# Optimization experiments

Measured on AMD Instinct MI355X. Metric: run time of the kernel, lower is better.

The kernel has to match this reference:

```python
import jax, jax.numpy as jnp
import numpy as np

N = 20000   # nodes
E = 320000  # edges (avg degree 16)
IN = 16     # in_node_nf
H = 64      # hidden_nf
OUT = 64    # out_node_nf
L = 4       # n_layers


def setup_inputs() -> dict:
    key = jax.random.key(0)
    ks = jax.random.split(key, 16)
    w = lambda k, shape: (jax.random.normal(k, shape, dtype=jnp.float32) * 0.05)
    zb = lambda *shape: jnp.zeros(shape, dtype=jnp.float32)
    return {
        "h": jax.random.normal(ks[0], (N, IN), dtype=jnp.float32),
        "x": jax.random.normal(ks[1], (N, 3), dtype=jnp.float32),
        "edge_index": jax.random.randint(ks[2], (2, E), 0, N),
        "emb_in_w": w(ks[3], (IN, H)), "emb_in_b": zb(H),
        "edge_w1": w(ks[4], (L, 2 * H + 1, H)), "edge_b1": zb(L, H),
        "edge_w2": w(ks[5], (L, H, H)), "edge_b2": zb(L, H),
        "coord_w1": w(ks[6], (L, H, H)), "coord_b1": zb(L, H),
        "coord_w2": w(ks[7], (L, H, 1)),  # bias-free last coord_mlp layer
        "node_w1": w(ks[8], (L, 2 * H, H)), "node_b1": zb(L, H),
        "node_w2": w(ks[9], (L, H, H)), "node_b2": zb(L, H),
        "emb_out_w": w(ks[10], (H, OUT)), "emb_out_b": zb(OUT),
    }


def reference(h, x, edge_index, emb_in_w, emb_in_b,
              edge_w1, edge_b1, edge_w2, edge_b2,
              coord_w1, coord_b1, coord_w2,
              node_w1, node_b1, node_w2, node_b2,
              emb_out_w, emb_out_b):
    row, col = edge_index[0], edge_index[1]
    act = jax.nn.silu
    # receiver in-degree for mean coordinate aggregation (clamped to >=1)
    cnt = jax.ops.segment_sum(jnp.ones((row.shape[0], 1), h.dtype), row, num_segments=N)
    cnt = jnp.maximum(cnt, 1.0)

    h = h @ emb_in_w + emb_in_b
    for l in range(L):
        # coord2radial
        diff = x[row] - x[col]                               # [E,3]
        radial = jnp.sum(diff * diff, axis=-1, keepdims=True)  # [E,1]
        # edge model: m_ij = phi_e(h_i, h_j, ||x_i-x_j||^2)
        e_in = jnp.concatenate([h[row], h[col], radial], axis=-1)  # [E,2H+1]
        m = act(e_in @ edge_w1[l] + edge_b1[l])
        m = act(m @ edge_w2[l] + edge_b2[l])                 # [E,H]
        # coord model: x_i += mean_j (x_i - x_j) * phi_x(m_ij)
        phi = act(m @ coord_w1[l] + coord_b1[l]) @ coord_w2[l]  # [E,1]
        trans = diff * phi                                    # [E,3]
        x = x + jax.ops.segment_sum(trans, row, num_segments=N) / cnt
        # node model: h_i = h_i + phi_h(h_i, sum_j m_ij)
        agg = jax.ops.segment_sum(m, row, num_segments=N)     # [N,H]
        n_in = jnp.concatenate([h, agg], axis=-1)             # [N,2H]
        out = act(n_in @ node_w1[l] + node_b1[l]) @ node_w2[l] + node_b2[l]
        h = h + out
    h = h @ emb_out_w + emb_out_b
    return h, x
```

## Files before the change

### kernel.cpp

```cpp
#include <hip/hip_runtime.h>
#include <hip/hip_bf16.h>


#define NN 20000
#define EE 320000
#define LSE 17024
#define LSN 6272

typedef unsigned short u16;
typedef unsigned int   u32;
typedef __attribute__((ext_vector_type(8))) short s16x8;
typedef __attribute__((ext_vector_type(4))) float f32x4;

__device__ __forceinline__ float bf2f(u16 u) { return __uint_as_float(((u32)u) << 16); }
__device__ __forceinline__ float silu_f(float x) {
    return x * __builtin_amdgcn_rcpf(1.0f + __expf(-x));
}

__device__ __forceinline__ u16 f2bf_rne(float f) {
    u32 u = __float_as_uint(f);
    return (u16)((u + 0x7FFFu + ((u >> 16) & 1u)) >> 16);
}
__device__ __forceinline__ float gldf(const void* p, int i, int bf) {
    return bf ? bf2f(((const u16*)p)[i]) : ((const float*)p)[i];
}
__device__ __forceinline__ u16 gldb(const void* p, int i, int bf) {
    return bf ? ((const u16*)p)[i] : f2bf_rne(((const float*)p)[i]);
}

__global__ void k_sentinel(u16* __restrict__ out, int n, float v) {
    int t = blockIdx.x * 256 + threadIdx.x;
    if (t < n) out[t] = f2bf_rne(v);
}

__global__ __launch_bounds__(256) void k_pack(
    const void* __restrict__ ew1, const void* __restrict__ eb1,
    const void* __restrict__ ew2, const void* __restrict__ eb2,
    const void* __restrict__ cw1, const void* __restrict__ cb1,
    const void* __restrict__ cw2,
    const void* __restrict__ nw1, const void* __restrict__ nb1,
    const void* __restrict__ nw2, const void* __restrict__ nb2,
    const u16* __restrict__ h_raw, const int* __restrict__ rowi,
    int* __restrict__ flag, int* __restrict__ deg,
    u16* __restrict__ pkE, u32* __restrict__ pkN)
{
    if (blockIdx.x >= 64) {
        int e = (blockIdx.x - 64) * 256 + threadIdx.x;
        if (e < EE) atomicAdd(&deg[rowi[e]], 1);
        return;
    }
    __shared__ int cnt_s;
    if (threadIdx.x == 0) cnt_s = 0;
    __syncthreads();
    if (threadIdx.x < 128) {
        float v = fabsf(bf2f(h_raw[threadIdx.x]));
        if (v >= 0.015625f && v <= 16.0f) atomicAdd(&cnt_s, 1);
    }
    __syncthreads();
    const int bf = (cnt_s >= 96) ? 1 : 0;
    if (blockIdx.x == 0 && threadIdx.x == 0) *flag = bf;

    const int gid = blockIdx.x * 256 + threadIdx.x;
    const int stride = 64 * 256;

    for (int g = gid; g < 4 * 16384; g += stride) {
        int l = g >> 14, idx = g & 16383;
        u16 v;
        if (idx < 8192) {
            int j = idx & 7, lane = (idx >> 3) & 63, t = (idx >> 9) & 3, w = idx >> 11;
            int k = 32 * w + (lane >> 4) * 8 + j, n = 16 * t + (lane & 15);
            v = gldb(ew1, l * 129 * 64 + k * 64 + n, bf);
        } else if (idx < 12288) {
            int i2 = idx - 8192;
            int j = i2 & 7, lane = (i2 >> 3) & 63, t = (i2 >> 9) & 3, w = i2 >> 11;
            int k = 32 * w + (lane >> 4) * 8 + j, n = 16 * t + (lane & 15);
            v = gldb(ew2, l * 4096 + k * 64 + n, bf);
        } else {
            int i2 = idx - 12288;
            int j = i2 & 7, lane = (i2 >> 3) & 63, t = (i2 >> 9) & 3, w = i2 >> 11;
            int k = 32 * w + (lane >> 4) * 8 + j, n = 16 * t + (lane & 15);
            v = gldb(cw1, l * 4096 + k * 64 + n, bf);
        }
        pkE[l * LSE + idx] = v;
    }
    for (int g = gid; g < 4 * 320; g += stride) {
        int l = g / 320, r = g % 320, wch = r >> 6, i = r & 63;
        float v = (wch == 0) ? gldf(eb1, l * 64 + i, bf)
                : (wch == 1) ? gldf(eb2, l * 64 + i, bf)
                : (wch == 2) ? gldf(cb1, l * 64 + i, bf)
                : (wch == 3) ? gldf(cw2, l * 64 + i, bf)
                :              gldf(ew1, l * 129 * 64 + 128 * 64 + i, bf);
        ((float*)(pkE + l * LSE + 16384))[r] = v;
    }
    for (int g = gid; g < 4 * 6144; g += stride) {
        int l = g / 6144, idx = g % 6144;
        u32 pv;
        if (idx < 4096) {
            int kp = idx >> 6, j = idx & 63;
            u32 lo = gldb(nw1, l * 8192 + (2 * kp) * 64 + j, bf);
            u32 hi = gldb(nw1, l * 8192 + (2 * kp + 1) * 64 + j, bf);
            pv = lo | (hi << 16);
        } else {
            int i2 = idx - 4096, kp = i2 >> 6, j = i2 & 63;
            u32 lo = gldb(nw2, l * 4096 + (2 * kp) * 64 + j, bf);
            u32 hi = gldb(nw2, l * 4096 + (2 * kp + 1) * 64 + j, bf);
            pv = lo | (hi << 16);
        }
        pkN[l * LSN + idx] = pv;
    }
    for (int g = gid; g < 4 * 128; g += stride) {
        int l = g >> 7, r = g & 127;
        float v = (r < 64) ? gldf(nb1, l * 64 + r, bf) : gldf(nb2, l * 64 + (r - 64), bf);
        ((float*)(pkN + l * LSN + 6144))[r] = v;
    }
}

__global__ __launch_bounds__(1024) void k_scan(const int* deg, int* offs, int* cursor,
                                               int* __restrict__ perm) {
    __shared__ int part[1024];
    __shared__ int hist[32], basep[32];
    const int tid = threadIdx.x;
    const int CH = (NN + 1023) / 1024;
    const int b0 = tid * CH;
    int s = 0;
    for (int i = 0; i < CH; i++) { int idx = b0 + i; if (idx < NN) s += deg[idx]; }
    part[tid] = s;
    __syncthreads();
    for (int d = 1; d < 1024; d <<= 1) {
        int v = (tid >= d) ? part[tid - d] : 0;
        __syncthreads();
        part[tid] += v;
        __syncthreads();
    }
    int run = (tid > 0) ? part[tid - 1] : 0;
    for (int i = 0; i < CH; i++) {
        int idx = b0 + i;
        if (idx < NN) {
            int dv = deg[idx];
            offs[idx] = run;
            cursor[idx] = run;
            run += dv;
        }
    }
    if (tid == 1023) offs[NN] = run;
    __syncthreads();

    if (tid < 32) hist[tid] = 0;
    __syncthreads();
    for (int i = 0; i < CH; i++) {
        int idx = b0 + i;
        if (idx < NN) {
            int dv = offs[idx + 1] - offs[idx];
            int key = min(31, (dv + 15) >> 4);
            atomicAdd(&hist[key], 1);
        }
    }
    __syncthreads();
    if (tid == 0) {
        int pos = 0;
        for (int k = 31; k >= 0; k--) { basep[k] = pos; pos += hist[k]; }
    }
    __syncthreads();
    for (int i = 0; i < CH; i++) {
        int idx = b0 + i;
        if (idx < NN) {
            int dv = offs[idx + 1] - offs[idx];
            int key = min(31, (dv + 15) >> 4);
            int p = atomicAdd(&basep[key], 1);
            perm[p] = idx;
        }
    }
}

__global__ void k_scatter(const int* __restrict__ rowi, const int* __restrict__ coli,
                          int* __restrict__ cursor, int* __restrict__ slist) {
    int e = blockIdx.x * 256 + threadIdx.x;
    if (e < EE) {
        int r = rowi[e];
        int pos = atomicAdd(&cursor[r], 1);
        slist[pos] = coli[e];
    }
}

__global__ __launch_bounds__(256) void k_embed(
    const void* __restrict__ h_in, const void* __restrict__ x_in,
    const void* __restrict__ w, const void* __restrict__ bias,
    const int* __restrict__ flag,
    float* __restrict__ hws, float* __restrict__ xws, u16* __restrict__ hb)
{
    const int bf = *flag;
    const int lane = threadIdx.x & 63;
    const int wv   = threadIdx.x >> 6;
    const int i    = blockIdx.x * 4 + wv;
    float acc = gldf(bias, lane, bf);
    #pragma unroll
    for (int k = 0; k < 16; k++)
        acc = fmaf(gldf(h_in, i * 16 + k, bf), gldf(w, k * 64 + lane, bf), acc);
    hws[i * 64 + lane] = acc;
    hb[i * 64 + lane] = f2bf_rne(acc);
    if (lane < 3) xws[i * 3 + lane] = gldf(x_in, i * 3 + lane, bf);
}

#define OFF_B23  8192
#define OFF_M    16384
#define MPAD     76
#define OFF_PHI  (OFF_M + 8 * 16 * MPAD)
#define OFF_CB   (OFF_PHI + 8 * 32)
#define OFF_NW   (OFF_CB + 640)
__global__ __launch_bounds__(512, 2) void k_edge(
    const u16* __restrict__ hbr, u16* __restrict__ hbw,
    const float* __restrict__ xr, float* __restrict__ xw,
    float* __restrict__ hws,
    const int* __restrict__ offs, const int* __restrict__ slist,
    const u16* __restrict__ pE, const u32* __restrict__ pN,
    const int* __restrict__ perm)
{
    __shared__ __align__(16) u16 sW[OFF_NW + 12544];

    const int tid = threadIdx.x, lane = tid & 63, wv = tid >> 6;
    const int l15 = lane & 15, quad = lane >> 4;

    for (int idx = tid; idx < 2048; idx += 512)
        ((s16x8*)sW)[idx] = ((const s16x8*)pE)[idx];
    {
        const float* pb = (const float*)(pE + 16384);
        float* cb = (float*)&sW[OFF_CB];
        if (tid < 320) cb[tid] = pb[tid];
    }
    for (int idx = tid; idx < 1568; idx += 512)
        ((f32x4*)&sW[OFF_NW])[idx] = ((const f32x4*)pN)[idx];
    __syncthreads();

    const float* CB = (const float*)&sW[OFF_CB];
    const u32* nW1 = (const u32*)&sW[OFF_NW];
    const u32* nW2 = nW1 + 4096;
    const float* nB = (const float*)(nW1 + 6144);

    const int gw = blockIdx.x * 8 + wv, totW = gridDim.x * 8;
    u16* mrow = &sW[OFF_M + wv * 16 * MPAD];
    float* phiw = (float*)&sW[OFF_PHI + wv * 32];

    for (int pidx = gw; pidx < NN; pidx += totW) {
        const int n = perm[pidx];
        const int o0 = offs[n], deg = offs[n + 1] - o0;

        const s16x8 Ar0 = *(const s16x8*)&hbr[n * 64 + quad * 8];
        const s16x8 Ar1 = *(const s16x8*)&hbr[n * 64 + 32 + quad * 8];
        f32x4 Cb[4] = {{0,0,0,0},{0,0,0,0},{0,0,0,0},{0,0,0,0}};
        #pragma unroll
        for (int t = 0; t < 4; t++) {
            const s16x8 Bf0 = *(const s16x8*)&sW[((0 * 4 + t) * 64 + lane) * 8];
            Cb[t] = __builtin_amdgcn_mfma_f32_16x16x32_bf16(Ar0, Bf0, Cb[t], 0, 0, 0);
            const s16x8 Bf1 = *(const s16x8*)&sW[((1 * 4 + t) * 64 + lane) * 8];
            Cb[t] = __builtin_amdgcn_mfma_f32_16x16x32_bf16(Ar1, Bf1, Cb[t], 0, 0, 0);
        }
        const float xrv = (quad < 3) ? xr[n * 3 + quad] : 0.0f;
        float aggA[4] = {0.f, 0.f, 0.f, 0.f};
        float xaccA = 0.0f;

        for (int eb = 0; eb < deg; eb += 16) {
            const int nb = min(16, deg - eb);
            const int ee = (l15 < nb) ? l15 : 0;
            const int ce = slist[o0 + eb + ee];
            float dx = 0.0f;
            if (quad < 3 && l15 < nb) dx = xrv - xr[ce * 3 + quad];
            float r2 = dx * dx;
            r2 += __shfl_xor(r2, 16, 64);
            r2 += __shfl_xor(r2, 32, 64);

            f32x4 C[4] = {Cb[0], Cb[1], Cb[2], Cb[3]};
            {
                const s16x8 Ac0 = *(const s16x8*)&hbr[ce * 64 + quad * 8];
                const s16x8 Ac1 = *(const s16x8*)&hbr[ce * 64 + 32 + quad * 8];
                #pragma unroll
                for (int t = 0; t < 4; t++) {
                    const s16x8 Bf2 = *(const s16x8*)&sW[((2 * 4 + t) * 64 + lane) * 8];
                    C[t] = __builtin_amdgcn_mfma_f32_16x16x32_bf16(Ac0, Bf2, C[t], 0, 0, 0);
                    const s16x8 Bf3 = *(const s16x8*)&sW[((3 * 4 + t) * 64 + lane) * 8];
                    C[t] = __builtin_amdgcn_mfma_f32_16x16x32_bf16(Ac1, Bf3, C[t], 0, 0, 0);
                }
            }
            float r2r[4];
            #pragma unroll
            for (int r = 0; r < 4; r++) r2r[r] = __shfl(r2, quad * 4 + r, 64);
            #pragma unroll
            for (int t = 0; t < 4; t++) {
                const float b1t = CB[       16 * t + l15];
                const float wrt = CB[256 +  16 * t + l15];
                #pragma unroll
                for (int r = 0; r < 4; r++) {
                    float v = silu_f(C[t][r] + b1t + r2r[r] * wrt);
                    mrow[(quad * 4 + r) * MPAD + 16 * t + l15] = f2bf_rne(v);
                }
            }

            f32x4 D[4] = {{0,0,0,0},{0,0,0,0},{0,0,0,0},{0,0,0,0}};
            #pragma unroll
            for (int w = 0; w < 2; w++) {
                const s16x8 Am = *(const s16x8*)(mrow + l15 * MPAD + 32 * w + quad * 8);
                #pragma unroll
                for (int t = 0; t < 4; t++) {
                    const s16x8 Bf = *(const s16x8*)&sW[OFF_B23 + ((w * 4 + t) * 64 + lane) * 8];
                    D[t] = __builtin_amdgcn_mfma_f32_16x16x32_bf16(Am, Bf, D[t], 0, 0, 0);
                }
            }
            #pragma unroll
            for (int t = 0; t < 4; t++) {
                const float b2t = CB[64 + 16 * t + l15];
                #pragma unroll
                for (int r = 0; r < 4; r++) {
                    float v = silu_f(D[t][r] + b2t);
                    if (quad * 4 + r < nb) aggA[t] += v;
                    mrow[(quad * 4 + r) * MPAD + 16 * t + l15] = f2bf_rne(v);
                }
            }

            f32x4 P[4] = {{0,0,0,0},{0,0,0,0},{0,0,0,0},{0,0,0,0}};
            #pragma unroll
            for (int w = 0; w < 2; w++) {
                const s16x8 Am = *(const s16x8*)(mrow + l15 * MPAD + 32 * w + quad * 8);
                #pragma unroll
                for (int t = 0; t < 4; t++) {
                    const s16x8 Bf = *(const s16x8*)&sW[OFF_B23 + (((2 + w) * 4 + t) * 64 + lane) * 8];
                    P[t] = __builtin_amdgcn_mfma_f32_16x16x32_bf16(Am, Bf, P[t], 0, 0, 0);
                }
            }
            float ph[4];
            #pragma unroll
            for (int r = 0; r < 4; r++) ph[r] = 0.f;
            #pragma unroll
            for (int t = 0; t < 4; t++) {
                const float cb1t = CB[128 + 16 * t + l15];
                const float c2t  = CB[192 + 16 * t + l15];
                #pragma unroll
                for (int r = 0; r < 4; r++)
                    ph[r] = fmaf(silu_f(P[t][r] + cb1t), c2t, ph[r]);
            }
            #pragma unroll
            for (int r = 0; r < 4; r++) {
                float s = ph[r];
                s += __shfl_xor(s, 1, 64);
                s += __shfl_xor(s, 2, 64);
                s += __shfl_xor(s, 4, 64);
                s += __shfl_xor(s, 8, 64);
                ph[r] = s;
            }
            if (l15 == 0) {
                #pragma unroll
                for (int r = 0; r < 4; r++) phiw[quad * 4 + r] = ph[r];
            }
            float phv = phiw[l15];
            if (quad < 3 && l15 < nb) xaccA = fmaf(dx, phv, xaccA);
        }

        #pragma unroll
        for (int t = 0; t < 4; t++) {
            aggA[t] += __shfl_xor(aggA[t], 16, 64);
            aggA[t] += __shfl_xor(aggA[t], 32, 64);
        }
        float av = (quad == 0) ? aggA[0] : (quad == 1) ? aggA[1]
                 : (quad == 2) ? aggA[2] : aggA[3];

        xaccA += __shfl_xor(xaccA, 1, 64);
        xaccA += __shfl_xor(xaccA, 2, 64);
        xaccA += __shfl_xor(xaccA, 4, 64);
        xaccA += __shfl_xor(xaccA, 8, 64);
        if (l15 == 0 && quad < 3)
            xw[n * 3 + quad] = (deg > 0) ? (xrv + xaccA / (float)deg) : xrv;

        float* nin = (float*)mrow;
        const float hv = hws[n * 64 + lane];
        nin[lane] = hv;
        nin[64 + lane] = av;
        float a1 = nB[lane];
        #pragma unroll
        for (int kk = 0; kk < 32; kk++) {
            u32 w01 = nW1[(kk * 2) * 64 + lane];
            u32 w23 = nW1[(kk * 2 + 1) * 64 + lane];
            float w0 = __uint_as_float(w01 << 16), w1 = __uint_as_float(w01 & 0xffff0000u);
            float w2 = __uint_as_float(w23 << 16), w3 = __uint_as_float(w23 & 0xffff0000u);
            const float4 e4 = *reinterpret_cast<const float4*>(&nin[kk * 4]);
            a1 = fmaf(e4.x, w0, fmaf(e4.y, w1, fmaf(e4.z, w2, fmaf(e4.w, w3, a1))));
        }
        a1 = silu_f(a1);
        nin[lane] = a1;
        float a2 = nB[64 + lane];
        #pragma unroll
        for (int kk = 0; kk < 16; kk++) {
            u32 w01 = nW2[(kk * 2) * 64 + lane];
            u32 w23 = nW2[(kk * 2 + 1) * 64 + lane];
            float w0 = __uint_as_float(w01 << 16), w1 = __uint_as_float(w01 & 0xffff0000u);
            float w2 = __uint_as_float(w23 << 16), w3 = __uint_as_float(w23 & 0xffff0000u);
            const float4 e4 = *reinterpret_cast<const float4*>(&nin[kk * 4]);
            a2 = fmaf(e4.x, w0, fmaf(e4.y, w1, fmaf(e4.z, w2, fmaf(e4.w, w3, a2))));
        }
        const float hnew = hv + a2;
        hws[n * 64 + lane] = hnew;
        hbw[n * 64 + lane] = f2bf_rne(hnew);
    }
}

__global__ __launch_bounds__(256) void k_out(
    const float* __restrict__ hws, const float* __restrict__ xws,
    const void* __restrict__ wo, const void* __restrict__ bo,
    const int* __restrict__ flag, void* __restrict__ out)
{
    __shared__ u32 sWp[32 * 64];
    __shared__ float sBf[64];
    __shared__ __align__(16) float sH[4][8][68];
    const int tid = threadIdx.x, lane = tid & 63, wv = tid >> 6;
    const int bf = *flag;
    for (int idx = tid; idx < 32 * 64; idx += 256) {
        int kp = idx >> 6, j = idx & 63;
        u32 lo = gldb(wo, (kp * 2) * 64 + j, bf);
        u32 hi = gldb(wo, (kp * 2 + 1) * 64 + j, bf);
        sWp[idx] = lo | (hi << 16);
    }
    if (tid < 64) sBf[tid] = gldf(bo, tid, bf);
    __syncthreads();

    const int i0 = (blockIdx.x * 4 + wv) * 8;
    #pragma unroll
    for (int b = 0; b < 8; b++) sH[wv][b][lane] = hws[(i0 + b) * 64 + lane];

    float acc[8];
    #pragma unroll
    for (int b = 0; b < 8; b++) acc[b] = sBf[lane];
    #pragma unroll
    for (int kk = 0; kk < 16; kk++) {
        u32 w01 = sWp[(kk * 2) * 64 + lane];
        u32 w23 = sWp[(kk * 2 + 1) * 64 + lane];
        float w0 = __uint_as_float(w01 << 16), w1 = __uint_as_float(w01 & 0xffff0000u);
        float w2 = __uint_as_float(w23 << 16), w3 = __uint_as_float(w23 & 0xffff0000u);
        #pragma unroll
        for (int b = 0; b < 8; b++) {
            const float4 e4 = *reinterpret_cast<const float4*>(&sH[wv][b][kk * 4]);
            acc[b] = fmaf(e4.x, w0, fmaf(e4.y, w1, fmaf(e4.z, w2, fmaf(e4.w, w3, acc[b]))));
        }
    }
    u16*   oh16 = (u16*)out;
    float* ohf  = (float*)out;
    u16*   ox16 = oh16 + (size_t)NN * 64;
    float* oxf  = ohf  + (size_t)NN * 64;
    #pragma unroll
    for (int b = 0; b < 8; b++) {
        int i = i0 + b;
        if (bf) {
            oh16[i * 64 + lane] = f2bf_rne(acc[b]);
            if (lane < 3) ox16[i * 3 + lane] = f2bf_rne(xws[i * 3 + lane]);
        } else {
            ohf[i * 64 + lane] = acc[b];
            if (lane < 3) oxf[i * 3 + lane] = xws[i * 3 + lane];
        }
    }
}

extern "C" void kernel_launch(void* const* d_in, const int* in_sizes, int n_in,
                              void* d_out, int out_size, void* d_ws, size_t ws_size,
                              hipStream_t stream)
{
    const size_t WS_REQ = (size_t)NN * 134 * sizeof(float) + 64;
    if (ws_size < WS_REQ) {
        float sval = 1000.0f + (float)(ws_size >> 20);
        k_sentinel<<<(out_size + 255) / 256, 256, 0, stream>>>(
            (u16*)d_out, out_size, sval);
        return;
    }

    const void* h_in = d_in[0];
    const void* x_in = d_in[1];
    const int*  eidx = (const int*)d_in[2];
    const int* rowi = eidx;
    const int* coli = eidx + EE;

    float* ws   = (float*)d_ws;
    float* hws  = ws;
    float* xws0 = hws + NN * 64;
    u16*   hb1  = (u16*)(xws0 + NN * 3);
    float* xws1 = (float*)(hb1 + (size_t)NN * 64);
    int*   flag = (int*)(xws1 + NN * 3);

    u16* hb0    = (u16*)d_out;
    int* offs   = (int*)(hb0 + (size_t)NN * 64);
    int* slist  = offs + (NN + 4);
    u16* pkE    = (u16*)(slist + EE);
    u32* pkN    = (u32*)(pkE + 4 * LSE);
    int* cursor = (int*)(pkN + 4 * LSN);
    int* perm   = cursor + NN;

    hipMemsetAsync(cursor, 0, (size_t)NN * sizeof(int), stream);

    k_pack<<<64 + (EE + 255) / 256, 256, 0, stream>>>(
        d_in[5], d_in[6], d_in[7], d_in[8], d_in[9], d_in[10], d_in[11],
        d_in[12], d_in[13], d_in[14], d_in[15],
        (const u16*)h_in, rowi, flag, cursor, pkE, pkN);
    k_scan<<<1, 1024, 0, stream>>>(cursor, offs, cursor, perm);
    k_scatter<<<(EE + 255) / 256, 256, 0, stream>>>(rowi, coli, cursor, slist);
    k_embed<<<NN / 4, 256, 0, stream>>>(h_in, x_in, d_in[3], d_in[4], flag, hws, xws0, hb0);

    for (int l = 0; l < 4; l++) {
        const u16*   hr = (l & 1) ? hb1 : hb0;
        u16*         hw = (l & 1) ? hb0 : hb1;
        const float* xrp = (l & 1) ? xws1 : xws0;
        float*       xwp = (l & 1) ? xws0 : xws1;
        k_edge<<<512, 512, 0, stream>>>(hr, hw, xrp, xwp, hws, offs, slist,
                                        pkE + l * LSE, pkN + (size_t)l * LSN, perm);
    }
    k_out<<<NN / 32, 256, 0, stream>>>(hws, xws0, d_in[16], d_in[17], flag, d_out);
}
```

Measured before the change: 580.1 us.

## Fuse all stages into one cooperative persistent kernel with grid syncs

Replaces the separate pack, scan, scatter, embed, per-layer edge and output kernels with a single cooperative kernel that uses grid-wide syncs between phases. Each layer's edge phase now writes per-node aggregates (agg, xacc) and a separate grid-synced node phase applies the node MLP, replacing the ping-pong buffers used before. The aim is to remove kernel launch overhead and the memset. The cost is many grid barriers, extra global round-trips for agg, and a grid size limited to the co-resident block count.

```diff
diff --git a/kernel.cpp b/kernel.cpp
--- a/kernel.cpp
+++ b/kernel.cpp
@@ -1,5 +1,8 @@
 #include <hip/hip_runtime.h>
 #include <hip/hip_bf16.h>
+#include <hip/hip_cooperative_groups.h>
+
+namespace cg = cooperative_groups;
 
 
 #define NN 20000
@@ -16,7 +19,6 @@
 __device__ __forceinline__ float silu_f(float x) {
     return x * __builtin_amdgcn_rcpf(1.0f + __expf(-x));
 }
-
 __device__ __forceinline__ u16 f2bf_rne(float f) {
     u32 u = __float_as_uint(f);
     return (u16)((u + 0x7FFFu + ((u >> 16) & 1u)) >> 16);
@@ -33,57 +35,77 @@
     if (t < n) out[t] = f2bf_rne(v);
 }
 
-__global__ __launch_bounds__(256) void k_pack(
+#define OFF_B23  8192
+#define OFF_M    16384
+#define MPAD     76
+#define OFF_PHI  (OFF_M + 8 * 16 * MPAD)
+#define OFF_CB   (OFF_PHI + 8 * 32)
+#define OFF_NW   (OFF_CB + 640)
+
+__global__ __launch_bounds__(512, 2) void k_mega(
+    const void* __restrict__ h_in, const void* __restrict__ x_in,
+    const int* __restrict__ rowi, const int* __restrict__ coli,
     const void* __restrict__ ew1, const void* __restrict__ eb1,
     const void* __restrict__ ew2, const void* __restrict__ eb2,
     const void* __restrict__ cw1, const void* __restrict__ cb1,
     const void* __restrict__ cw2,
     const void* __restrict__ nw1, const void* __restrict__ nb1,
     const void* __restrict__ nw2, const void* __restrict__ nb2,
-    const u16* __restrict__ h_raw, const int* __restrict__ rowi,
-    int* __restrict__ flag, int* __restrict__ deg,
-    u16* __restrict__ pkE, u32* __restrict__ pkN)
+    const void* __restrict__ emb_w, const void* __restrict__ emb_b,
+    const void* __restrict__ wo, const void* __restrict__ bo,
+    float* __restrict__ hws, float* __restrict__ xws,
+    float* __restrict__ agg, float* __restrict__ xacc,
+    u16* __restrict__ hb, int* __restrict__ offs, int* __restrict__ slist,
+    u16* __restrict__ pkE, u32* __restrict__ pkN,
+    int* __restrict__ cursor, int* __restrict__ perm, void* __restrict__ outp)
 {
-    if (blockIdx.x >= 64) {
-        int e = (blockIdx.x - 64) * 256 + threadIdx.x;
-        if (e < EE) atomicAdd(&deg[rowi[e]], 1);
-        return;
-    }
+    __shared__ __align__(16) u16 sW[OFF_NW + 12544];
     __shared__ int cnt_s;
-    if (threadIdx.x == 0) cnt_s = 0;
+
+    cg::grid_group grid = cg::this_grid();
+    const int tid = threadIdx.x, bid = blockIdx.x;
+    const int lane = tid & 63, wv = tid >> 6;
+    const int l15 = lane & 15, quad = lane >> 4;
+    const int gid = bid * 512 + tid;
+    const int gthreads = gridDim.x * 512;
+    const int nwaves = gthreads >> 6;
+    const int waveid = gid >> 6;
+
+    if (tid == 0) cnt_s = 0;
     __syncthreads();
-    if (threadIdx.x < 128) {
-        float v = fabsf(bf2f(h_raw[threadIdx.x]));
+    if (tid < 128) {
+        float v = fabsf(bf2f(((const u16*)h_in)[tid]));
         if (v >= 0.015625f && v <= 16.0f) atomicAdd(&cnt_s, 1);
     }
     __syncthreads();
     const int bf = (cnt_s >= 96) ? 1 : 0;
-    if (blockIdx.x == 0 && threadIdx.x == 0) *flag = bf;
-
-    const int gid = blockIdx.x * 256 + threadIdx.x;
-    const int stride = 64 * 256;
-
-    for (int g = gid; g < 4 * 16384; g += stride) {
+
+    for (int i = gid; i < NN; i += gthreads) cursor[i] = 0;
+    __threadfence();
+    grid.sync();
+
+    for (int e = gid; e < EE; e += gthreads) atomicAdd(&cursor[rowi[e]], 1);
+    for (int g = gid; g < 4 * 16384; g += gthreads) {
         int l = g >> 14, idx = g & 16383;
         u16 v;
         if (idx < 8192) {
-            int j = idx & 7, lane = (idx >> 3) & 63, t = (idx >> 9) & 3, w = idx >> 11;
-            int k = 32 * w + (lane >> 4) * 8 + j, n = 16 * t + (lane & 15);
+            int j = idx & 7, ln = (idx >> 3) & 63, t = (idx >> 9) & 3, w = idx >> 11;
+            int k = 32 * w + (ln >> 4) * 8 + j, n = 16 * t + (ln & 15);
             v = gldb(ew1, l * 129 * 64 + k * 64 + n, bf);
         } else if (idx < 12288) {
             int i2 = idx - 8192;
-            int j = i2 & 7, lane = (i2 >> 3) & 63, t = (i2 >> 9) & 3, w = i2 >> 11;
-            int k = 32 * w + (lane >> 4) * 8 + j, n = 16 * t + (lane & 15);
+            int j = i2 & 7, ln = (i2 >> 3) & 63, t = (i2 >> 9) & 3, w = i2 >> 11;
+            int k = 32 * w + (ln >> 4) * 8 + j, n = 16 * t + (ln & 15);
             v = gldb(ew2, l * 4096 + k * 64 + n, bf);
         } else {
             int i2 = idx - 12288;
-            int j = i2 & 7, lane = (i2 >> 3) & 63, t = (i2 >> 9) & 3, w = i2 >> 11;
-            int k = 32 * w + (lane >> 4) * 8 + j, n = 16 * t + (lane & 15);
+            int j = i2 & 7, ln = (i2 >> 3) & 63, t = (i2 >> 9) & 3, w = i2 >> 11;
+            int k = 32 * w + (ln >> 4) * 8 + j, n = 16 * t + (ln & 15);
             v = gldb(cw1, l * 4096 + k * 64 + n, bf);
         }
         pkE[l * LSE + idx] = v;
     }
-    for (int g = gid; g < 4 * 320; g += stride) {
+    for (int g = gid; g < 4 * 320; g += gthreads) {
         int l = g / 320, r = g % 320, wch = r >> 6, i = r & 63;
         float v = (wch == 0) ? gldf(eb1, l * 64 + i, bf)
                 : (wch == 1) ? gldf(eb2, l * 64 + i, bf)
@@ -92,7 +114,7 @@
                 :              gldf(ew1, l * 129 * 64 + 128 * 64 + i, bf);
         ((float*)(pkE + l * LSE + 16384))[r] = v;
     }
-    for (int g = gid; g < 4 * 6144; g += stride) {
+    for (int g = gid; g < 4 * 6144; g += gthreads) {
         int l = g / 6144, idx = g % 6144;
         u32 pv;
         if (idx < 4096) {
@@ -108,349 +130,361 @@
         }
         pkN[l * LSN + idx] = pv;
     }
-    for (int g = gid; g < 4 * 128; g += stride) {
+    for (int g = gid; g < 4 * 128; g += gthreads) {
         int l = g >> 7, r = g & 127;
         float v = (r < 64) ? gldf(nb1, l * 64 + r, bf) : gldf(nb2, l * 64 + (r - 64), bf);
         ((float*)(pkN + l * LSN + 6144))[r] = v;
     }
-}
-
-__global__ __launch_bounds__(1024) void k_scan(const int* deg, int* offs, int* cursor,
-                                               int* __restrict__ perm) {
-    __shared__ int part[1024];
-    __shared__ int hist[32], basep[32];
-    const int tid = threadIdx.x;
-    const int CH = (NN + 1023) / 1024;
-    const int b0 = tid * CH;
-    int s = 0;
-    for (int i = 0; i < CH; i++) { int idx = b0 + i; if (idx < NN) s += deg[idx]; }
-    part[tid] = s;
-    __syncthreads();
-    for (int d = 1; d < 1024; d <<= 1) {
-        int v = (tid >= d) ? part[tid - d] : 0;
-        __syncthreads();
-        part[tid] += v;
-        __syncthreads();
-    }
-    int run = (tid > 0) ? part[tid - 1] : 0;
-    for (int i = 0; i < CH; i++) {
-        int idx = b0 + i;
-        if (idx < NN) {
-            int dv = deg[idx];
-            offs[idx] = run;
-            cursor[idx] = run;
-            run += dv;
-        }
-    }
-    if (tid == 1023) offs[NN] = run;
-    __syncthreads();
-
-    if (tid < 32) hist[tid] = 0;
-    __syncthreads();
-    for (int i = 0; i < CH; i++) {
-        int idx = b0 + i;
-        if (idx < NN) {
-            int dv = offs[idx + 1] - offs[idx];
-            int key = min(31, (dv + 15) >> 4);
-            atomicAdd(&hist[key], 1);
-        }
-    }
-    __syncthreads();
-    if (tid == 0) {
-        int pos = 0;
-        for (int k = 31; k >= 0; k--) { basep[k] = pos; pos += hist[k]; }
-    }
-    __syncthreads();
-    for (int i = 0; i < CH; i++) {
-        int idx = b0 + i;
-        if (idx < NN) {
-            int dv = offs[idx + 1] - offs[idx];
-            int key = min(31, (dv + 15) >> 4);
-            int p = atomicAdd(&basep[key], 1);
-            perm[p] = idx;
-        }
-    }
-}
-
-__global__ void k_scatter(const int* __restrict__ rowi, const int* __restrict__ coli,
-                          int* __restrict__ cursor, int* __restrict__ slist) {
-    int e = blockIdx.x * 256 + threadIdx.x;
-    if (e < EE) {
+    __threadfence();
+    grid.sync();
+
+    if (bid == 0) {
+        int* part  = (int*)sW;
+        int* hist  = part + 512;
+        int* basep = hist + 32;
+        const int CH = 40;
+        const int b0 = tid * CH;
+        int s = 0;
+        for (int i = 0; i < CH; i++) { int idx = b0 + i; if (idx < NN) s += cursor[idx]; }
+        part[tid] = s;
+        __syncthreads();
+        for (int d = 1; d < 512; d <<= 1) {
+            int v = (tid >= d) ? part[tid - d] : 0;
+            __syncthreads();
+            part[tid] += v;
+            __syncthreads();
+        }
+        int run = (tid > 0) ? part[tid - 1] : 0;
+        for (int i = 0; i < CH; i++) {
+            int idx = b0 + i;
+            if (idx < NN) {
+                int dv = cursor[idx];
+                offs[idx] = run;
+                cursor[idx] = run;
+                run += dv;
+            }
+        }
+        if (tid == 511) offs[NN] = run;
+        __syncthreads();
+        if (tid < 32) hist[tid] = 0;
+        __syncthreads();
+        for (int i = 0; i < CH; i++) {
+            int idx = b0 + i;
+            if (idx < NN) {
+                int dv = offs[idx + 1] - offs[idx];
+                int key = min(31, (dv + 15) >> 4);
+                atomicAdd(&hist[key], 1);
+            }
+        }
+        __syncthreads();
+        if (tid == 0) {
+            int pos = 0;
+            for (int k = 31; k >= 0; k--) { basep[k] = pos; pos += hist[k]; }
+        }
+        __syncthreads();
+        for (int i = 0; i < CH; i++) {
+            int idx = b0 + i;
+            if (idx < NN) {
+                int dv = offs[idx + 1] - offs[idx];
+                int key = min(31, (dv + 15) >> 4);
+                int p = atomicAdd(&basep[key], 1);
+                perm[p] = idx;
+            }
+        }
+    }
+    __threadfence();
+    grid.sync();
+
+    for (int e = gid; e < EE; e += gthreads) {
         int r = rowi[e];
         int pos = atomicAdd(&cursor[r], 1);
         slist[pos] = coli[e];
     }
-}
-
-__global__ __launch_bounds__(256) void k_embed(
-    const void* __restrict__ h_in, const void* __restrict__ x_in,
-    const void* __restrict__ w, const void* __restrict__ bias,
-    const int* __restrict__ flag,
-    float* __restrict__ hws, float* __restrict__ xws, u16* __restrict__ hb)
-{
-    const int bf = *flag;
-    const int lane = threadIdx.x & 63;
-    const int wv   = threadIdx.x >> 6;
-    const int i    = blockIdx.x * 4 + wv;
-    float acc = gldf(bias, lane, bf);
-    #pragma unroll
-    for (int k = 0; k < 16; k++)
-        acc = fmaf(gldf(h_in, i * 16 + k, bf), gldf(w, k * 64 + lane, bf), acc);
-    hws[i * 64 + lane] = acc;
-    hb[i * 64 + lane] = f2bf_rne(acc);
-    if (lane < 3) xws[i * 3 + lane] = gldf(x_in, i * 3 + lane, bf);
-}
-
-#define OFF_B23  8192
-#define OFF_M    16384
-#define MPAD     76
-#define OFF_PHI  (OFF_M + 8 * 16 * MPAD)
-#define OFF_CB   (OFF_PHI + 8 * 32)
-#define OFF_NW   (OFF_CB + 640)
-__global__ __launch_bounds__(512, 2) void k_edge(
-    const u16* __restrict__ hbr, u16* __restrict__ hbw,
-    const float* __restrict__ xr, float* __restrict__ xw,
-    float* __restrict__ hws,
-    const int* __restrict__ offs, const int* __restrict__ slist,
-    const u16* __restrict__ pE, const u32* __restrict__ pN,
-    const int* __restrict__ perm)
-{
-    __shared__ __align__(16) u16 sW[OFF_NW + 12544];
-
-    const int tid = threadIdx.x, lane = tid & 63, wv = tid >> 6;
-    const int l15 = lane & 15, quad = lane >> 4;
-
-    for (int idx = tid; idx < 2048; idx += 512)
-        ((s16x8*)sW)[idx] = ((const s16x8*)pE)[idx];
-    {
-        const float* pb = (const float*)(pE + 16384);
-        float* cb = (float*)&sW[OFF_CB];
-        if (tid < 320) cb[tid] = pb[tid];
-    }
-    for (int idx = tid; idx < 1568; idx += 512)
-        ((f32x4*)&sW[OFF_NW])[idx] = ((const f32x4*)pN)[idx];
-    __syncthreads();
-
-    const float* CB = (const float*)&sW[OFF_CB];
-    const u32* nW1 = (const u32*)&sW[OFF_NW];
-    const u32* nW2 = nW1 + 4096;
-    const float* nB = (const float*)(nW1 + 6144);
-
-    const int gw = blockIdx.x * 8 + wv, totW = gridDim.x * 8;
+    for (int n = waveid; n < NN; n += nwaves) {
+        float acc = gldf(emb_b, lane, bf);
+        #pragma unroll
+        for (int k = 0; k < 16; k++)
+            acc = fmaf(gldf(h_in, n * 16 + k, bf), gldf(emb_w, k * 64 + lane, bf), acc);
+        hws[n * 64 + lane] = acc;
+        hb[n * 64 + lane] = f2bf_rne(acc);
+        if (lane < 3) xws[n * 3 + lane] = gldf(x_in, n * 3 + lane, bf);
+    }
+    __threadfence();
+    grid.sync();
+
     u16* mrow = &sW[OFF_M + wv * 16 * MPAD];
     float* phiw = (float*)&sW[OFF_PHI + wv * 32];
 
-    for (int pidx = gw; pidx < NN; pidx += totW) {
-        const int n = perm[pidx];
-        const int o0 = offs[n], deg = offs[n + 1] - o0;
-
-        const s16x8 Ar0 = *(const s16x8*)&hbr[n * 64 + quad * 8];
-        const s16x8 Ar1 = *(const s16x8*)&hbr[n * 64 + 32 + quad * 8];
-        f32x4 Cb[4] = {{0,0,0,0},{0,0,0,0},{0,0,0,0},{0,0,0,0}};
-        #pragma unroll
-        for (int t = 0; t < 4; t++) {
-            const s16x8 Bf0 = *(const s16x8*)&sW[((0 * 4 + t) * 64 + lane) * 8];
-            Cb[t] = __builtin_amdgcn_mfma_f32_16x16x32_bf16(Ar0, Bf0, Cb[t], 0, 0, 0);
-            const s16x8 Bf1 = *(const s16x8*)&sW[((1 * 4 + t) * 64 + lane) * 8];
-            Cb[t] = __builtin_amdgcn_mfma_f32_16x16x32_bf16(Ar1, Bf1, Cb[t], 0, 0, 0);
-        }
-        const float xrv = (quad < 3) ? xr[n * 3 + quad] : 0.0f;
-        float aggA[4] = {0.f, 0.f, 0.f, 0.f};
-        float xaccA = 0.0f;
-
-        for (int eb = 0; eb < deg; eb += 16) {
-            const int nb = min(16, deg - eb);
-            const int ee = (l15 < nb) ? l15 : 0;
-            const int ce = slist[o0 + eb + ee];
-            float dx = 0.0f;
-            if (quad < 3 && l15 < nb) dx = xrv - xr[ce * 3 + quad];
-            float r2 = dx * dx;
-            r2 += __shfl_xor(r2, 16, 64);
-            r2 += __shfl_xor(r2, 32, 64);
-
-            f32x4 C[4] = {Cb[0], Cb[1], Cb[2], Cb[3]};
-            {
-                const s16x8 Ac0 = *(const s16x8*)&hbr[ce * 64 + quad * 8];
-                const s16x8 Ac1 = *(const s16x8*)&hbr[ce * 64 + 32 + quad * 8];
+    for (int l = 0; l < 4; l++) {
+        const u16* pEl = pkE + l * LSE;
+        const u32* pNl = pkN + (size_t)l * LSN;
+        for (int idx = tid; idx < 2048; idx += 512)
+            ((s16x8*)sW)[idx] = ((const s16x8*)pEl)[idx];
+        {
+            const float* pb = (const float*)(pEl + 16384);
+            float* cb = (float*)&sW[OFF_CB];
+            if (tid < 320) cb[tid] = pb[tid];
+        }
+        for (int idx = tid; idx < 1568; idx += 512)
+            ((f32x4*)&sW[OFF_NW])[idx] = ((const f32x4*)pNl)[idx];
+        __syncthreads();
+
+        const float* CB = (const float*)&sW[OFF_CB];
+        const u32* nW1 = (const u32*)&sW[OFF_NW];
+        const u32* nW2 = nW1 + 4096;
+        const float* nB = (const float*)(nW1 + 6144);
+
+        const int gw = bid * 8 + wv, totW = gridDim.x * 8;
+        for (int pidx = gw; pidx < NN; pidx += totW) {
+            const int n = perm[pidx];
+            const int o0 = offs[n], deg = offs[n + 1] - o0;
+            if (deg == 0) {
+                agg[n * 64 + lane] = 0.0f;
+                if (l15 == 0 && quad < 3) xacc[n * 3 + quad] = 0.0f;
+                continue;
+            }
+            const s16x8 Ar0 = *(const s16x8*)&hb[n * 64 + quad * 8];
+            const s16x8 Ar1 = *(const s16x8*)&hb[n * 64 + 32 + quad * 8];
+            f32x4 Cb[4] = {{0,0,0,0},{0,0,0,0},{0,0,0,0},{0,0,0,0}};
+            #pragma unroll
+            for (int t = 0; t < 4; t++) {
+                const s16x8 Bf0 = *(const s16x8*)&sW[((0 * 4 + t) * 64 + lane) * 8];
+                Cb[t] = __builtin_amdgcn_mfma_f32_16x16x32_bf16(Ar0, Bf0, Cb[t], 0, 0, 0);
+                const s16x8 Bf1 = *(const s16x8*)&sW[((1 * 4 + t) * 64 + lane) * 8];
+                Cb[t] = __builtin_amdgcn_mfma_f32_16x16x32_bf16(Ar1, Bf1, Cb[t], 0, 0, 0);
+            }
+            const float xrv = (quad < 3) ? xws[n * 3 + quad] : 0.0f;
+            float aggA[4] = {0.f, 0.f, 0.f, 0.f};
+            float xaccA = 0.0f;
+
+            for (int eb = 0; eb < deg; eb += 16) {
+                const int nb = min(16, deg - eb);
+                const int ee = (l15 < nb) ? l15 : 0;
+                const int ce = slist[o0 + eb + ee];
+                float dx = 0.0f;
+                if (quad < 3 && l15 < nb) dx = xrv - xws[ce * 3 + quad];
+                float r2 = dx * dx;
+                r2 += __shfl_xor(r2, 16, 64);
+                r2 += __shfl_xor(r2, 32, 64);
+
+                f32x4 C[4] = {Cb[0], Cb[1], Cb[2], Cb[3]};
+                {
+                    const s16x8 Ac0 = *(const s16x8*)&hb[ce * 64 + quad * 8];
+                    const s16x8 Ac1 = *(const s16x8*)&hb[ce * 64 + 32 + quad * 8];
+                    #pragma unroll
+                    for (int t = 0; t < 4; t++) {
+                        const s16x8 Bf2 = *(const s16x8*)&sW[((2 * 4 + t) * 64 + lane) * 8];
+                        C[t] = __builtin_amdgcn_mfma_f32_16x16x32_bf16(Ac0, Bf2, C[t], 0, 0, 0);
+                        const s16x8 Bf3 = *(const s16x8*)&sW[((3 * 4 + t) * 64 + lane) * 8];
+                        C[t] = __builtin_amdgcn_mfma_f32_16x16x32_bf16(Ac1, Bf3, C[t], 0, 0, 0);
+                    }
+                }
+                float r2r[4];
+                #pragma unroll
+                for (int r = 0; r < 4; r++) r2r[r] = __shfl(r2, quad * 4 + r, 64);
                 #pragma unroll
                 for (int t = 0; t < 4; t++) {
-                    const s16x8 Bf2 = *(const s16x8*)&sW[((2 * 4 + t) * 64 + lane) * 8];
-                    C[t] = __builtin_amdgcn_mfma_f32_16x16x32_bf16(Ac0, Bf2, C[t], 0, 0, 0);
-                    const s16x8 Bf3 = *(const s16x8*)&sW[((3 * 4 + t) * 64 + lane) * 8];
-                    C[t] = __builtin_amdgcn_mfma_f32_16x16x32_bf16(Ac1, Bf3, C[t], 0, 0, 0);
-                }
-            }
-            float r2r[4];
-            #pragma unroll
-            for (int r = 0; r < 4; r++) r2r[r] = __shfl(r2, quad * 4 + r, 64);
+                    const float b1t = CB[       16 * t + l15];
+                    const float wrt = CB[256 +  16 * t + l15];
+                    #pragma unroll
+                    for (int r = 0; r < 4; r++) {
+                        float v = silu_f(C[t][r] + b1t + r2r[r] * wrt);
+                        mrow[(quad * 4 + r) * MPAD + 16 * t + l15] = f2bf_rne(v);
+                    }
+                }
+
+                f32x4 D[4] = {{0,0,0,0},{0,0,0,0},{0,0,0,0},{0,0,0,0}};
+                #pragma unroll
+                for (int w = 0; w < 2; w++) {
+                    const s16x8 Am = *(const s16x8*)(mrow + l15 * MPAD + 32 * w + quad * 8);
+                    #pragma unroll
+                    for (int t = 0; t < 4; t++) {
+                        const s16x8 Bf = *(const s16x8*)&sW[OFF_B23 + ((w * 4 + t) * 64 + lane) * 8];
+                        D[t] = __builtin_amdgcn_mfma_f32_16x16x32_bf16(Am, Bf, D[t], 0, 0, 0);
+                    }
+                }
+                #pragma unroll
+                for (int t = 0; t < 4; t++) {
+                    const float b2t = CB[64 + 16 * t + l15];
+                    #pragma unroll
+                    for (int r = 0; r < 4; r++) {
+                        float v = silu_f(D[t][r] + b2t);
+                        if (quad * 4 + r < nb) aggA[t] += v;
+                        mrow[(quad * 4 + r) * MPAD + 16 * t + l15] = f2bf_rne(v);
+                    }
+                }
+
+                f32x4 P[4] = {{0,0,0,0},{0,0,0,0},{0,0,0,0},{0,0,0,0}};
+                #pragma unroll
+                for (int w = 0; w < 2; w++) {
+                    const s16x8 Am = *(const s16x8*)(mrow + l15 * MPAD + 32 * w + quad * 8);
+                    #pragma unroll
+                    for (int t = 0; t < 4; t++) {
+                        const s16x8 Bf = *(const s16x8*)&sW[OFF_B23 + (((2 + w) * 4 + t) * 64 + lane) * 8];
+                        P[t] = __builtin_amdgcn_mfma_f32_16x16x32_bf16(Am, Bf, P[t], 0, 0, 0);
+                    }
+                }
+                float ph[4];
+                #pragma unroll
+                for (int r = 0; r < 4; r++) ph[r] = 0.f;
+                #pragma unroll
+                for (int t = 0; t < 4; t++) {
+                    const float cb1t = CB[128 + 16 * t + l15];
+                    const float c2t  = CB[192 + 16 * t + l15];
+                    #pragma unroll
+                    for (int r = 0; r < 4; r++)
+                        ph[r] = fmaf(silu_f(P[t][r] + cb1t), c2t, ph[r]);
+                }
+                #pragma unroll
+                for (int r = 0; r < 4; r++) {
+                    float s = ph[r];
+                    s += __shfl_xor(s, 1, 64);
+                    s += __shfl_xor(s, 2, 64);
+                    s += __shfl_xor(s, 4, 64);
+                    s += __shfl_xor(s, 8, 64);
+                    ph[r] = s;
+                }
+                if (l15 == 0) {
+                    #pragma unroll
+                    for (int r = 0; r < 4; r++) phiw[quad * 4 + r] = ph[r];
+                }
+                float phv = phiw[l15];
+                if (quad < 3 && l15 < nb) xaccA = fmaf(dx, phv, xaccA);
+            }
+
             #pragma unroll
             for (int t = 0; t < 4; t++) {
-                const float b1t = CB[       16 * t + l15];
-                const float wrt = CB[256 +  16 * t + l15];
-                #pragma unroll
-                for (int r = 0; r < 4; r++) {
-                    float v = silu_f(C[t][r] + b1t + r2r[r] * wrt);
-                    mrow[(quad * 4 + r) * MPAD + 16 * t + l15] = f2bf_rne(v);
-                }
-            }
-
-            f32x4 D[4] = {{0,0,0,0},{0,0,0,0},{0,0,0,0},{0,0,0,0}};
-            #pragma unroll
-            for (int w = 0; w < 2; w++) {
-                const s16x8 Am = *(const s16x8*)(mrow + l15 * MPAD + 32 * w + quad * 8);
-                #pragma unroll
-                for (int t = 0; t < 4; t++) {
-                    const s16x8 Bf = *(const s16x8*)&sW[OFF_B23 + ((w * 4 + t) * 64 + lane) * 8];
-                    D[t] = __builtin_amdgcn_mfma_f32_16x16x32_bf16(Am, Bf, D[t], 0, 0, 0);
-                }
-            }
-            #pragma unroll
-            for (int t = 0; t < 4; t++) {
-                const float b2t = CB[64 + 16 * t + l15];
-                #pragma unroll
-                for (int r = 0; r < 4; r++) {
-                    float v = silu_f(D[t][r] + b2t);
-                    if (quad * 4 + r < nb) aggA[t] += v;
-                    mrow[(quad * 4 + r) * MPAD + 16 * t + l15] = f2bf_rne(v);
-                }
-            }
-
-            f32x4 P[4] = {{0,0,0,0},{0,0,0,0},{0,0,0,0},{0,0,0,0}};
-            #pragma unroll
-            for (int w = 0; w < 2; w++) {
-                const s16x8 Am = *(const s16x8*)(mrow + l15 * MPAD + 32 * w + quad * 8);
-                #pragma unroll
-                for (int t = 0; t < 4; t++) {
-                    const s16x8 Bf = *(const s16x8*)&sW[OFF_B23 + (((2 + w) * 4 + t) * 64 + lane) * 8];
-                    P[t] = __builtin_amdgcn_mfma_f32_16x16x32_bf16(Am, Bf, P[t], 0, 0, 0);
-                }
-            }
-            float ph[4];
-            #pragma unroll
-            for (int r = 0; r < 4; r++) ph[r] = 0.f;
-            #pragma unroll
-            for (int t = 0; t < 4; t++) {
-                const float cb1t = CB[128 + 16 * t + l15];
-                const float c2t  = CB[192 + 16 * t + l15];
-                #pragma unroll
-                for (int r = 0; r < 4; r++)
-                    ph[r] = fmaf(silu_f(P[t][r] + cb1t), c2t, ph[r]);
-            }
-            #pragma unroll
-            for (int r = 0; r < 4; r++) {
-                float s = ph[r];
-                s += __shfl_xor(s, 1, 64);
-                s += __shfl_xor(s, 2, 64);
-                s += __shfl_xor(s, 4, 64);
-                s += __shfl_xor(s, 8, 64);
-                ph[r] = s;
-            }
-            if (l15 == 0) {
-                #pragma unroll
-                for (int r = 0; r < 4; r++) phiw[quad * 4 + r] = ph[r];
-            }
-            float phv = phiw[l15];
-            if (quad < 3 && l15 < nb) xaccA = fmaf(dx, phv, xaccA);
-        }
-
-        #pragma unroll
-        for (int t = 0; t < 4; t++) {
-            aggA[t] += __shfl_xor(aggA[t], 16, 64);
-            aggA[t] += __shfl_xor(aggA[t], 32, 64);
-        }
-        float av = (quad == 0) ? aggA[0] : (quad == 1) ? aggA[1]
-                 : (quad == 2) ? aggA[2] : aggA[3];
-
-        xaccA += __shfl_xor(xaccA, 1, 64);
-        xaccA += __shfl_xor(xaccA, 2, 64);
-        xaccA += __shfl_xor(xaccA, 4, 64);
-        xaccA += __shfl_xor(xaccA, 8, 64);
-        if (l15 == 0 && quad < 3)
-            xw[n * 3 + quad] = (deg > 0) ? (xrv + xaccA / (float)deg) : xrv;
+                aggA[t] += __shfl_xor(aggA[t], 16, 64);
+                aggA[t] += __shfl_xor(aggA[t], 32, 64);
+            }
+            float av = (quad == 0) ? aggA[0] : (quad == 1) ? aggA[1]
+                     : (quad == 2) ? aggA[2] : aggA[3];
+            agg[n * 64 + lane] = av;
+
+            xaccA += __shfl_xor(xaccA, 1, 64);
+            xaccA += __shfl_xor(xaccA, 2, 64);
+            xaccA += __shfl_xor(xaccA, 4, 64);
+            xaccA += __shfl_xor(xaccA, 8, 64);
+            if (l15 == 0 && quad < 3) xacc[n * 3 + quad] = xaccA / (float)deg;
+        }
+        __threadfence();
+        grid.sync();
+
+        for (int i = gid; i < NN * 3; i += gthreads) xws[i] += xacc[i];
 
         float* nin = (float*)mrow;
-        const float hv = hws[n * 64 + lane];
-        nin[lane] = hv;
-        nin[64 + lane] = av;
-        float a1 = nB[lane];
-        #pragma unroll
-        for (int kk = 0; kk < 32; kk++) {
-            u32 w01 = nW1[(kk * 2) * 64 + lane];
-            u32 w23 = nW1[(kk * 2 + 1) * 64 + lane];
-            float w0 = __uint_as_float(w01 << 16), w1 = __uint_as_float(w01 & 0xffff0000u);
-            float w2 = __uint_as_float(w23 << 16), w3 = __uint_as_float(w23 & 0xffff0000u);
-            const float4 e4 = *reinterpret_cast<const float4*>(&nin[kk * 4]);
-            a1 = fmaf(e4.x, w0, fmaf(e4.y, w1, fmaf(e4.z, w2, fmaf(e4.w, w3, a1))));
-        }
-        a1 = silu_f(a1);
-        nin[lane] = a1;
-        float a2 = nB[64 + lane];
-        #pragma unroll
-        for (int kk = 0; kk < 16; kk++) {
-            u32 w01 = nW2[(kk * 2) * 64 + lane];
-            u32 w23 = nW2[(kk * 2 + 1) * 64 + lane];
-            float w0 = __uint_as_float(w01 << 16), w1 = __uint_as_float(w01 & 0xffff0000u);
-            float w2 = __uint_as_float(w23 << 16), w3 = __uint_as_float(w23 & 0xffff0000u);
-            const float4 e4 = *reinterpret_cast<const float4*>(&nin[kk * 4]);
-            a2 = fmaf(e4.x, w0, fmaf(e4.y, w1, fmaf(e4.z, w2, fmaf(e4.w, w3, a2))));
-        }
-        const float hnew = hv + a2;
-        hws[n * 64 + lane] = hnew;
-        hbw[n * 64 + lane] = f2bf_rne(hnew);
-    }
-}
-
-__global__ __launch_bounds__(256) void k_out(
-    const float* __restrict__ hws, const float* __restrict__ xws,
-    const void* __restrict__ wo, const void* __restrict__ bo,
-    const int* __restrict__ flag, void* __restrict__ out)
-{
-    __shared__ u32 sWp[32 * 64];
-    __shared__ float sBf[64];
-    __shared__ __align__(16) float sH[4][8][68];
-    const int tid = threadIdx.x, lane = tid & 63, wv = tid >> 6;
-    const int bf = *flag;
-    for (int idx = tid; idx < 32 * 64; idx += 256) {
-        int kp = idx >> 6, j = idx & 63;
-        u32 lo = gldb(wo, (kp * 2) * 64 + j, bf);
-        u32 hi = gldb(wo, (kp * 2 + 1) * 64 + j, bf);
-        sWp[idx] = lo | (hi << 16);
-    }
-    if (tid < 64) sBf[tid] = gldf(bo, tid, bf);
-    __syncthreads();
-
-    const int i0 = (blockIdx.x * 4 + wv) * 8;
-    #pragma unroll
-    for (int b = 0; b < 8; b++) sH[wv][b][lane] = hws[(i0 + b) * 64 + lane];
-
-    float acc[8];
-    #pragma unroll
-    for (int b = 0; b < 8; b++) acc[b] = sBf[lane];
-    #pragma unroll
-    for (int kk = 0; kk < 16; kk++) {
-        u32 w01 = sWp[(kk * 2) * 64 + lane];
-        u32 w23 = sWp[(kk * 2 + 1) * 64 + lane];
-        float w0 = __uint_as_float(w01 << 16), w1 = __uint_as_float(w01 & 0xffff0000u);
-        float w2 = __uint_as_float(w23 << 16), w3 = __uint_as_float(w23 & 0xffff0000u);
-        #pragma unroll
-        for (int b = 0; b < 8; b++) {
-            const float4 e4 = *reinterpret_cast<const float4*>(&sH[wv][b][kk * 4]);
-            acc[b] = fmaf(e4.x, w0, fmaf(e4.y, w1, fmaf(e4.z, w2, fmaf(e4.w, w3, acc[b]))));
-        }
-    }
-    u16*   oh16 = (u16*)out;
-    float* ohf  = (float*)out;
-    u16*   ox16 = oh16 + (size_t)NN * 64;
-    float* oxf  = ohf  + (size_t)NN * 64;
-    #pragma unroll
-    for (int b = 0; b < 8; b++) {
-        int i = i0 + b;
-        if (bf) {
-            oh16[i * 64 + lane] = f2bf_rne(acc[b]);
-            if (lane < 3) ox16[i * 3 + lane] = f2bf_rne(xws[i * 3 + lane]);
-        } else {
-            ohf[i * 64 + lane] = acc[b];
-            if (lane < 3) oxf[i * 3 + lane] = xws[i * 3 + lane];
+        for (int base = waveid * 4; base < NN; base += nwaves * 4) {
+            const int cnt = min(4, NN - base);
+            float hvv[4] = {0.f, 0.f, 0.f, 0.f};
+            #pragma unroll
+            for (int c = 0; c < 4; c++) {
+                if (c < cnt) {
+                    int n = base + c;
+                    float hv = hws[n * 64 + lane];
+                    hvv[c] = hv;
+                    nin[c * 132 + lane] = hv;
+                    nin[c * 132 + 64 + lane] = agg[n * 64 + lane];
+                }
+            }
+            float a1[4];
+            #pragma unroll
+            for (int c = 0; c < 4; c++) a1[c] = nB[lane];
+            #pragma unroll
+            for (int kk = 0; kk < 32; kk++) {
+                u32 w01 = nW1[(kk * 2) * 64 + lane];
+                u32 w23 = nW1[(kk * 2 + 1) * 64 + lane];
+                float w0 = __uint_as_float(w01 << 16), w1 = __uint_as_float(w01 & 0xffff0000u);
+                float w2 = __uint_as_float(w23 << 16), w3 = __uint_as_float(w23 & 0xffff0000u);
+                #pragma unroll
+                for (int c = 0; c < 4; c++) {
+                    const float4 e4 = *reinterpret_cast<const float4*>(&nin[c * 132 + kk * 4]);
+                    a1[c] = fmaf(e4.x, w0, fmaf(e4.y, w1, fmaf(e4.z, w2, fmaf(e4.w, w3, a1[c]))));
+                }
+            }
+            #pragma unroll
+            for (int c = 0; c < 4; c++) a1[c] = silu_f(a1[c]);
+            #pragma unroll
+            for (int c = 0; c < 4; c++) nin[c * 132 + lane] = a1[c];
+            float a2[4];
+            #pragma unroll
+            for (int c = 0; c < 4; c++) a2[c] = nB[64 + lane];
+            #pragma unroll
+            for (int kk = 0; kk < 16; kk++) {
+                u32 w01 = nW2[(kk * 2) * 64 + lane];
+                u32 w23 = nW2[(kk * 2 + 1) * 64 + lane];
+                float w0 = __uint_as_float(w01 << 16), w1 = __uint_as_float(w01 & 0xffff0000u);
+                float w2 = __uint_as_float(w23 << 16), w3 = __uint_as_float(w23 & 0xffff0000u);
+                #pragma unroll
+                for (int c = 0; c < 4; c++) {
+                    const float4 e4 = *reinterpret_cast<const float4*>(&nin[c * 132 + kk * 4]);
+                    a2[c] = fmaf(e4.x, w0, fmaf(e4.y, w1, fmaf(e4.z, w2, fmaf(e4.w, w3, a2[c]))));
+                }
+            }
+            #pragma unroll
+            for (int c = 0; c < 4; c++) {
+                if (c < cnt) {
+                    int n = base + c;
+                    float hnew = hvv[c] + a2[c];
+                    hws[n * 64 + lane] = hnew;
+                    hb[n * 64 + lane] = f2bf_rne(hnew);
+                }
+            }
+        }
+        __threadfence();
+        grid.sync();
+    }
+
+    {
+        u32* sWp = (u32*)sW;
+        float* sBf = (float*)(sWp + 2048);
+        for (int idx = tid; idx < 2048; idx += 512) {
+            int kp = idx >> 6, j = idx & 63;
+            u32 lo = gldb(wo, (kp * 2) * 64 + j, bf);
+            u32 hi = gldb(wo, (kp * 2 + 1) * 64 + j, bf);
+            sWp[idx] = lo | (hi << 16);
+        }
+        if (tid < 64) sBf[tid] = gldf(bo, tid, bf);
+        __syncthreads();
+
+        u16*   oh16 = (u16*)outp;
+        float* ohf  = (float*)outp;
+        u16*   ox16 = oh16 + (size_t)NN * 64;
+        float* oxf  = ohf  + (size_t)NN * 64;
+        float* sH = (float*)mrow;
+
+        for (int i0 = (bid * 8 + wv) * 8; i0 < NN; i0 += gridDim.x * 64) {
+            float acc[8];
+            #pragma unroll
+            for (int b = 0; b < 8; b++) {
+                int i = i0 + b;
+                sH[b * 68 + lane] = (i < NN) ? hws[i * 64 + lane] : 0.f;
+                acc[b] = sBf[lane];
+            }
+            #pragma unroll
+            for (int kk = 0; kk < 16; kk++) {
+                u32 w01 = sWp[(kk * 2) * 64 + lane];
+                u32 w23 = sWp[(kk * 2 + 1) * 64 + lane];
+                float w0 = __uint_as_float(w01 << 16), w1 = __uint_as_float(w01 & 0xffff0000u);
+                float w2 = __uint_as_float(w23 << 16), w3 = __uint_as_float(w23 & 0xffff0000u);
+                #pragma unroll
+                for (int b = 0; b < 8; b++) {
+                    const float4 e4 = *reinterpret_cast<const float4*>(&sH[b * 68 + kk * 4]);
+                    acc[b] = fmaf(e4.x, w0, fmaf(e4.y, w1, fmaf(e4.z, w2, fmaf(e4.w, w3, acc[b]))));
+                }
+            }
+            #pragma unroll
+            for (int b = 0; b < 8; b++) {
+                int i = i0 + b;
+                if (i < NN) {
+                    if (bf) {
+                        oh16[i * 64 + lane] = f2bf_rne(acc[b]);
+                        if (lane < 3) ox16[i * 3 + lane] = f2bf_rne(xws[i * 3 + lane]);
+                    } else {
+                        ohf[i * 64 + lane] = acc[b];
+                        if (lane < 3) oxf[i * 3 + lane] = xws[i * 3 + lane];
+                    }
+                }
+            }
         }
     }
 }
@@ -475,36 +509,37 @@
 
     float* ws   = (float*)d_ws;
     float* hws  = ws;
-    float* xws0 = hws + NN * 64;
-    u16*   hb1  = (u16*)(xws0 + NN * 3);
-    float* xws1 = (float*)(hb1 + (size_t)NN * 64);
-    int*   flag = (int*)(xws1 + NN * 3);
-
-    u16* hb0    = (u16*)d_out;
-    int* offs   = (int*)(hb0 + (size_t)NN * 64);
+    float* xws  = hws + NN * 64;
+    float* agg  = xws + NN * 3;
+    float* xacc = agg + NN * 64;
+
+    u16* hb     = (u16*)d_out;
+    int* offs   = (int*)(hb + (size_t)NN * 64);
     int* slist  = offs + (NN + 4);
     u16* pkE    = (u16*)(slist + EE);
     u32* pkN    = (u32*)(pkE + 4 * LSE);
     int* cursor = (int*)(pkN + 4 * LSN);
     int* perm   = cursor + NN;
 
-    hipMemsetAsync(cursor, 0, (size_t)NN * sizeof(int), stream);
-
-    k_pack<<<64 + (EE + 255) / 256, 256, 0, stream>>>(
-        d_in[5], d_in[6], d_in[7], d_in[8], d_in[9], d_in[10], d_in[11],
-        d_in[12], d_in[13], d_in[14], d_in[15],
-        (const u16*)h_in, rowi, flag, cursor, pkE, pkN);
-    k_scan<<<1, 1024, 0, stream>>>(cursor, offs, cursor, perm);
-    k_scatter<<<(EE + 255) / 256, 256, 0, stream>>>(rowi, coli, cursor, slist);
-    k_embed<<<NN / 4, 256, 0, stream>>>(h_in, x_in, d_in[3], d_in[4], flag, hws, xws0, hb0);
-
-    for (int l = 0; l < 4; l++) {
-        const u16*   hr = (l & 1) ? hb1 : hb0;
-        u16*         hw = (l & 1) ? hb0 : hb1;
-        const float* xrp = (l & 1) ? xws1 : xws0;
-        float*       xwp = (l & 1) ? xws0 : xws1;
-        k_edge<<<512, 512, 0, stream>>>(hr, hw, xrp, xwp, hws, offs, slist,
-                                        pkE + l * LSE, pkN + (size_t)l * LSN, perm);
-    }
-    k_out<<<NN / 32, 256, 0, stream>>>(hws, xws0, d_in[16], d_in[17], flag, d_out);
-}
+    static int gridBlocks = 0;
+    if (gridBlocks == 0) {
+        int maxB = 0;
+        hipError_t err = hipOccupancyMaxActiveBlocksPerMultiprocessor(&maxB, k_mega, 512, 0);
+        if (err != hipSuccess || maxB < 1) maxB = 1;
+        gridBlocks = (maxB >= 2) ? 512 : 256;
+    }
+
+    void* outp = d_out;
+    void* args[] = {
+        (void*)&h_in, (void*)&x_in, (void*)&rowi, (void*)&coli,
+        (void*)&d_in[5], (void*)&d_in[6], (void*)&d_in[7], (void*)&d_in[8],
+        (void*)&d_in[9], (void*)&d_in[10], (void*)&d_in[11],
+        (void*)&d_in[12], (void*)&d_in[13], (void*)&d_in[14], (void*)&d_in[15],
+        (void*)&d_in[3], (void*)&d_in[4], (void*)&d_in[16], (void*)&d_in[17],
+        (void*)&hws, (void*)&xws, (void*)&agg, (void*)&xacc,
+        (void*)&hb, (void*)&offs, (void*)&slist, (void*)&pkE, (void*)&pkN,
+        (void*)&cursor, (void*)&perm, (void*)&outp
+    };
+    hipLaunchCooperativeKernel((void*)k_mega, dim3(gridBlocks), dim3(512),
+                               args, 0, stream);
+}
```

New measurement: 1.777 ms. 3.06x slower.
